# Performance work log

Hardware: AMD Instinct MI355X
Metric: run time of the kernel (lower is better)

The kernel has to match this reference:

```python
import jax, jax.numpy as jnp
import numpy as np

N = 4096  # matrix dimension; M=N, useFrame=False => nCols=N, nThetas=N*(N-1)/2


def _schedule(n):
    """Round-robin tournament schedule: n-1 rounds of n/2 disjoint (i,j) pairs
    covering all i<j exactly once, plus the canonical row-major theta index
    t(i,j) = i*n - i*(i+1)/2 + (j-i-1)."""
    assert n % 2 == 0
    ks = np.arange(1, n // 2)
    i_rounds, j_rounds, t_rounds = [], [], []
    for r in range(n - 1):
        a = np.concatenate(([n - 1], (r + ks) % (n - 1)))
        b = np.concatenate(([r % (n - 1)], (r - ks) % (n - 1)))
        i = np.minimum(a, b)
        j = np.maximum(a, b)
        t = i * n - (i * (i + 1)) // 2 + (j - i - 1)
        i_rounds.append(i)
        j_rounds.append(j)
        t_rounds.append(t)
    return (np.stack(i_rounds).astype(np.int32),
            np.stack(j_rounds).astype(np.int32),
            np.stack(t_rounds).astype(np.int32))


def setup_inputs() -> dict:
    key = jax.random.key(0)
    n_thetas = N * (N - 1) // 2
    # torch.nn.init.uniform_(thetas, 0, 2*pi)
    thetas = jax.random.uniform(key, (n_thetas,), jnp.float32, 0.0, 2.0 * float(np.pi))
    ri, rj, rt = _schedule(N)
    return {
        "thetas": thetas,
        "round_i": jnp.asarray(ri),      # [N-1, N/2]
        "round_j": jnp.asarray(rj),      # [N-1, N/2]
        "round_theta": jnp.asarray(rt),  # [N-1, N/2]
    }


def reference(thetas, round_i, round_j, round_theta):
    # Compose all N(N-1)/2 Givens rotations into U (left-multiplying identity).
    # Within each tournament round the N/2 pairs are disjoint, so rotations
    # commute and can be applied as one vectorized 2-row update.
    n = round_i.shape[0] + 1
    th = thetas[round_theta]            # [R, n/2]
    cs = jnp.cos(th)
    sn = jnp.sin(th)
    U0 = jnp.eye(n, dtype=thetas.dtype)

    def step(U, xs):
        i, j, c, s = xs                 # each [n/2] (c,s) or [n/2] int (i,j)
        Ui = U[i]                       # [n/2, n]
        Uj = U[j]                       # [n/2, n]
        U = U.at[i].set(c[:, None] * Ui - s[:, None] * Uj)
        U = U.at[j].set(s[:, None] * Ui + c[:, None] * Uj)
        return U, None

    U, _ = jax.lax.scan(step, U0, (round_i, round_j, cs, sn))
    return U  # nCols = N (useFrame=False) -> full matrix
```

## Files before the change

### kernel.cpp

```cpp
#include <hip/hip_runtime.h>
#include <math.h>

#define NDIM 4096
#define NR   4095
#define NPAIRS 2048
#define CB   8
#define NTHREADS 256
#define NWAVES (NTHREADS / 64)
#define TPT  8

__global__ void cs_precompute(const float* __restrict__ thetas,
                              const int* __restrict__ round_theta,
                              float2* __restrict__ cs, int total) {
    int idx = blockIdx.x * blockDim.x + threadIdx.x;
    if (idx >= total) return;
    int r = idx / NPAIRS;
    int k = idx - r * NPAIRS;
    float th = thetas[round_theta[idx]];
    float s, c;
    sincosf(th, &s, &c);
    if (k > 0 && k <= r && r < NR - k) s = -s;
    cs[idx] = make_float2(c, s);
}

#define XBAR()                                                          \
  { asm volatile("s_waitcnt lgkmcnt(0)" ::: "memory");                  \
    __builtin_amdgcn_s_barrier(); }

#define PIN8(A, U)                                                      \
    asm volatile("" :: "v"(A[U][0]), "v"(A[U][1]), "v"(A[U][2]),        \
                       "v"(A[U][3]), "v"(A[U][4]), "v"(A[U][5]),        \
                       "v"(A[U][6]), "v"(A[U][7]))

#define PINALL()                                                        \
  { PIN8(T, 0); PIN8(T, 1); PIN8(T, 2); PIN8(T, 3);                     \
    PIN8(T, 4); PIN8(T, 5); PIN8(T, 6); PIN8(T, 7);                     \
    PIN8(B, 0); PIN8(B, 1); PIN8(B, 2); PIN8(B, 3);                     \
    PIN8(B, 4); PIN8(B, 5); PIN8(B, 6); PIN8(B, 7); }

#define UPD(U, P, CC, SS)                                                     \
  { const float c_ = (CC), s_ = (SS);                                         \
    _Pragma("unroll") for (int c = 0; c < CB; ++c) {                          \
      float a = T[((U) + (P)) & 7][c], b = B[((U) - (P) + 8) & 7][c];         \
      T[((U) + (P)) & 7][c] = fmaf(c_, a, -(s_ * b));                         \
      B[((U) - (P) + 8) & 7][c] = fmaf(s_, a, c_ * b); } }

#define PHASE(P, RND, BUF, DO_PF)                                             \
  {                                                                           \
    PINALL();                                                                 \
    float na0[CB], nb0[CB], nbL[CB];                                          \
    {             \
      const float c_ = BUF[0].x, s_ = BUF[0].y;                               \
      _Pragma("unroll") for (int c = 0; c < CB; ++c) {                        \
        float a = T[(P) & 7][c], b = B[(0 - (P) + 8) & 7][c];                 \
        na0[c] = fmaf(c_, a, -(s_ * b));                                      \
        nb0[c] = fmaf(s_, a, c_ * b); } }                                     \
    float t7[CB];                                                             \
    _Pragma("unroll") for (int c = 0; c < CB; ++c)                            \
      t7[c] = __shfl_down(na0[c], 1);       \
    UPD(1, P, BUF[0].z, BUF[0].w)                                             \
    UPD(2, P, BUF[1].x, BUF[1].y)                                             \
    UPD(3, P, BUF[1].z, BUF[1].w)                                             \
    UPD(4, P, BUF[2].x, BUF[2].y)                                             \
    UPD(5, P, BUF[2].z, BUF[2].w)                                             \
    UPD(6, P, BUF[3].x, BUF[3].y)                                             \
    {                                \
      const float c_ = BUF[3].z, s_ = BUF[3].w;                               \
      _Pragma("unroll") for (int c = 0; c < CB; ++c) {                        \
        float a = T[(7 + (P)) & 7][c], b = B[(7 - (P) + 8) & 7][c];           \
        T[(7 + (P)) & 7][c] = fmaf(c_, a, -(s_ * b));                         \
        nbL[c] = fmaf(s_, a, c_ * b); } }                                     \
    if (DO_PF) {     \
      const float4* pf_ = csp + (size_t)((RND) + 2) * (NPAIRS / 2);           \
      BUF[0] = pf_[0]; BUF[1] = pf_[1]; BUF[2] = pf_[2]; BUF[3] = pf_[3];     \
    }                                                                         \
    float bi[CB];                                                             \
    _Pragma("unroll") for (int c = 0; c < CB; ++c)                            \
      bi[c] = __shfl_up(nbL[c], 1);                                           \
    if (lane == 0) { _Pragma("unroll") for (int c = 0; c < CB; ++c)           \
        naBuf[(P) & 1][wave][c] = na0[c]; }                                   \
    if (lane == 63) { _Pragma("unroll") for (int c = 0; c < CB; ++c)          \
        nbBuf[(P) & 1][wave][c] = nbL[c]; }                                   \
    XBAR();                                                                   \
    if (lane == 63) {                                                         \
      if (wave < NWAVES - 1) { _Pragma("unroll")                              \
        for (int c = 0; c < CB; ++c) t7[c] = naBuf[(P) & 1][wave + 1][c]; }   \
      else { _Pragma("unroll")                                                \
        for (int c = 0; c < CB; ++c) t7[c] = nbL[c]; } }                      \
    if (lane == 0 && wave > 0) { _Pragma("unroll")                            \
      for (int c = 0; c < CB; ++c) bi[c] = nbBuf[(P) & 1][wave - 1][c]; }     \
    _Pragma("unroll") for (int c = 0; c < CB; ++c) {                          \
      T[(P) & 7][c] = t7[c];                             \
      B[(0 - (P) + 8) & 7][c] = (tid == 0) ? na0[c] : nb0[c];                 \
      B[(7 - (P) + 8) & 7][c] = (tid == 0) ? nb0[c] : bi[c];                  \
    }                                                                         \
  }

__global__ __launch_bounds__(NTHREADS, 2)
void rotmat_systolic(const float2* __restrict__ cs,
                     float* __restrict__ out) {
    __shared__ float naBuf[2][NWAVES][CB];
    __shared__ float nbBuf[2][NWAVES][CB];

    const int tid  = threadIdx.x;
    const int lane = tid & 63;
    const int wave = tid >> 6;
    const int col0 = blockIdx.x * CB;

    float T[TPT][CB], B[TPT][CB];
#pragma unroll
    for (int u = 0; u < TPT; ++u) {
        int g = tid * TPT + u;
        int rowB = NR - g;
#pragma unroll
        for (int c = 0; c < CB; ++c) {
            T[u][c] = (g == col0 + c) ? 1.f : 0.f;
            B[u][c] = (rowB == col0 + c) ? 1.f : 0.f;
        }
    }

    const float4* csp = (const float4*)cs + (size_t)tid * (TPT / 2);
    float4 csbE[4], csbO[4];
    { const float4* p = csp;
      csbE[0] = p[0]; csbE[1] = p[1]; csbE[2] = p[2]; csbE[3] = p[3]; }
    { const float4* p = csp + (size_t)1 * (NPAIRS / 2);
      csbO[0] = p[0]; csbO[1] = p[1]; csbO[2] = p[2]; csbO[3] = p[3]; }

    int r = 0;
    for (int it = 0; it < 511; ++it, r += 8) {
        PHASE(0, r,     csbE, 1)
        PHASE(1, r + 1, csbO, 1)
        PHASE(2, r + 2, csbE, 1)
        PHASE(3, r + 3, csbO, 1)
        PHASE(4, r + 4, csbE, 1)
        PHASE(5, r + 5, csbO, 1)
        PHASE(6, r + 6, csbE, 1)
        PHASE(7, r + 7, csbO, 1)
    }
    PHASE(0, r,     csbE, 1)
    PHASE(1, r + 1, csbO, 1)
    PHASE(2, r + 2, csbE, 1)
    PHASE(3, r + 3, csbO, 1)
    PHASE(4, r + 4, csbE, 1)
    PHASE(5, r + 5, csbO, 0)
    PHASE(6, r + 6, csbE, 0)

#pragma unroll
    for (int u = 0; u < TPT; ++u) {
        int g = tid * TPT + u;
        int rowB = NR - g;
        float* Tp = T[(u + 7) & 7];
        float* Bp = B[(u + 1) & 7];
        float4* oT = (float4*)&out[(size_t)g * NDIM + col0];
        oT[0] = make_float4(Tp[0], Tp[1], Tp[2], Tp[3]);
        oT[1] = make_float4(Tp[4], Tp[5], Tp[6], Tp[7]);
        float4* oB = (float4*)&out[(size_t)rowB * NDIM + col0];
        oB[0] = make_float4(Bp[0], Bp[1], Bp[2], Bp[3]);
        oB[1] = make_float4(Bp[4], Bp[5], Bp[6], Bp[7]);
    }
}

extern "C" void kernel_launch(void* const* d_in, const int* in_sizes, int n_in,
                              void* d_out, int out_size, void* d_ws, size_t ws_size,
                              hipStream_t stream) {
    const float* thetas      = (const float*)d_in[0];
    const int*   round_theta = (const int*)d_in[3];
    float*       out         = (float*)d_out;

    const int total = NR * NPAIRS;
    float2* cs = (float2*)d_ws;

    cs_precompute<<<(total + 255) / 256, 256, 0, stream>>>(
        thetas, round_theta, cs, total);
    rotmat_systolic<<<NDIM / CB, NTHREADS, 0, stream>>>(cs, out);
}
```

Before: 4.104 ms.

## Overlap cross-wave halo exchange with compute by recomputing boundary rotations locally

Boundary lanes now read the neighbouring wave's values from shared memory at the start of each phase, before the barrier-dependent work. They then recompute the halo rotation locally using a prefetched cos/sin pair and the saved previous value. The barrier moves to the end of the phase, after the next round's boundary values are written, so the LDS round trip is no longer on the critical path between the edge rotations and the shuffle fixup. This costs extra registers (prevX, hst, hcs), a per-phase scalar cos/sin load for the edge lanes, and more complex boundary logic that could be wrong.

New measurement: 15.47 ms. 277% more time.

```diff
diff --git a/kernel.cpp b/kernel.cpp
--- a/kernel.cpp
+++ b/kernel.cpp
@@ -45,9 +45,16 @@
       T[((U) + (P)) & 7][c] = fmaf(c_, a, -(s_ * b));                         \
       B[((U) - (P) + 8) & 7][c] = fmaf(s_, a, c_ * b); } }
 
-#define PHASE(P, RND, BUF, DO_PF)                                             \
+#define PHASE(P, RND, BUF, DO_PF, DO_PH)                                      \
   {                                                                           \
     PINALL();                                                                 \
+    float hst[CB];      \
+    if (lane == 63 && wave < NWAVES - 1) {                                    \
+      _Pragma("unroll") for (int c = 0; c < CB; ++c)                          \
+        hst[c] = naS[(RND) & 1][wave + 1][c]; }                               \
+    if (lane == 0 && wave > 0) {                                              \
+      _Pragma("unroll") for (int c = 0; c < CB; ++c)                          \
+        hst[c] = nbS[(RND) & 1][wave - 1][c]; }                               \
     float na0[CB], nb0[CB], nbL[CB];                                          \
     {             \
       const float c_ = BUF[0].x, s_ = BUF[0].y;                               \
@@ -55,52 +62,58 @@
         float a = T[(P) & 7][c], b = B[(0 - (P) + 8) & 7][c];                 \
         na0[c] = fmaf(c_, a, -(s_ * b));                                      \
         nb0[c] = fmaf(s_, a, c_ * b); } }                                     \
-    float t7[CB];                                                             \
-    _Pragma("unroll") for (int c = 0; c < CB; ++c)                            \
-      t7[c] = __shfl_down(na0[c], 1);       \
+    {                          \
+      const float c_ = BUF[3].z, s_ = BUF[3].w;                               \
+      _Pragma("unroll") for (int c = 0; c < CB; ++c) {                        \
+        float a = T[(7 + (P)) & 7][c], b = B[(7 - (P) + 8) & 7][c];           \
+        T[(7 + (P)) & 7][c] = fmaf(c_, a, -(s_ * b));                         \
+        nbL[c] = fmaf(s_, a, c_ * b); } }                                     \
+    float t7[CB], bi[CB];                                                     \
+    _Pragma("unroll") for (int c = 0; c < CB; ++c) {                          \
+      t7[c] = __shfl_down(na0[c], 1);                                         \
+      bi[c] = __shfl_up(nbL[c], 1); }                                         \
+    if (lane == 63) {                       \
+      _Pragma("unroll") for (int c = 0; c < CB; ++c)                          \
+        t7[c] = (wave == NWAVES - 1) ? nbL[c]                                 \
+                : fmaf(hcs.x, hst[c], -(hcs.y * prevX[c])); }                 \
+    if (lane == 0 && wave > 0) {            \
+      _Pragma("unroll") for (int c = 0; c < CB; ++c)                          \
+        bi[c] = fmaf(hcs.y, prevX[c], hcs.x * hst[c]); }                      \
     UPD(1, P, BUF[0].z, BUF[0].w)                                             \
     UPD(2, P, BUF[1].x, BUF[1].y)                                             \
     UPD(3, P, BUF[1].z, BUF[1].w)                                             \
     UPD(4, P, BUF[2].x, BUF[2].y)                                             \
     UPD(5, P, BUF[2].z, BUF[2].w)                                             \
     UPD(6, P, BUF[3].x, BUF[3].y)                                             \
-    {                                \
-      const float c_ = BUF[3].z, s_ = BUF[3].w;                               \
-      _Pragma("unroll") for (int c = 0; c < CB; ++c) {                        \
-        float a = T[(7 + (P)) & 7][c], b = B[(7 - (P) + 8) & 7][c];           \
-        T[(7 + (P)) & 7][c] = fmaf(c_, a, -(s_ * b));                         \
-        nbL[c] = fmaf(s_, a, c_ * b); } }                                     \
-    if (DO_PF) {     \
+    if (DO_PF) {                \
       const float4* pf_ = csp + (size_t)((RND) + 2) * (NPAIRS / 2);           \
       BUF[0] = pf_[0]; BUF[1] = pf_[1]; BUF[2] = pf_[2]; BUF[3] = pf_[3];     \
     }                                                                         \
-    float bi[CB];                                                             \
+    float2 hn;                                                                \
+    if (DO_PH) { if (lane == 0 || lane == 63)                                 \
+        hn = cs2[(size_t)((RND) + 1) * NPAIRS + hidx]; }                      \
     _Pragma("unroll") for (int c = 0; c < CB; ++c)                            \
-      bi[c] = __shfl_up(nbL[c], 1);                                           \
-    if (lane == 0) { _Pragma("unroll") for (int c = 0; c < CB; ++c)           \
-        naBuf[(P) & 1][wave][c] = na0[c]; }                                   \
-    if (lane == 63) { _Pragma("unroll") for (int c = 0; c < CB; ++c)          \
-        nbBuf[(P) & 1][wave][c] = nbL[c]; }                                   \
-    XBAR();                                                                   \
-    if (lane == 63) {                                                         \
-      if (wave < NWAVES - 1) { _Pragma("unroll")                              \
-        for (int c = 0; c < CB; ++c) t7[c] = naBuf[(P) & 1][wave + 1][c]; }   \
-      else { _Pragma("unroll")                                                \
-        for (int c = 0; c < CB; ++c) t7[c] = nbL[c]; } }                      \
-    if (lane == 0 && wave > 0) { _Pragma("unroll")                            \
-      for (int c = 0; c < CB; ++c) bi[c] = nbBuf[(P) & 1][wave - 1][c]; }     \
+      prevX[c] = (lane == 0) ? na0[c] : nbL[c];                               \
     _Pragma("unroll") for (int c = 0; c < CB; ++c) {                          \
       T[(P) & 7][c] = t7[c];                             \
       B[(0 - (P) + 8) & 7][c] = (tid == 0) ? na0[c] : nb0[c];                 \
       B[(7 - (P) + 8) & 7][c] = (tid == 0) ? nb0[c] : bi[c];                  \
     }                                                                         \
+    if (lane == 0) {                \
+      _Pragma("unroll") for (int c = 0; c < CB; ++c)                          \
+        naS[((RND) + 1) & 1][wave][c] = T[(1 + (P)) & 7][c]; }                \
+    if (lane == 63) {               \
+      _Pragma("unroll") for (int c = 0; c < CB; ++c)                          \
+        nbS[((RND) + 1) & 1][wave][c] = B[(6 - (P) + 8) & 7][c]; }            \
+    if (DO_PH) hcs = hn;                                                      \
+    XBAR();                                                                   \
   }
 
 __global__ __launch_bounds__(NTHREADS, 2)
 void rotmat_systolic(const float2* __restrict__ cs,
                      float* __restrict__ out) {
-    __shared__ float naBuf[2][NWAVES][CB];
-    __shared__ float nbBuf[2][NWAVES][CB];
+    __shared__ float naS[2][NWAVES][CB];
+    __shared__ float nbS[2][NWAVES][CB];
 
     const int tid  = threadIdx.x;
     const int lane = tid & 63;
@@ -120,30 +133,54 @@
     }
 
     const float4* csp = (const float4*)cs + (size_t)tid * (TPT / 2);
+    const float2* cs2 = cs;
     float4 csbE[4], csbO[4];
     { const float4* p = csp;
       csbE[0] = p[0]; csbE[1] = p[1]; csbE[2] = p[2]; csbE[3] = p[3]; }
     { const float4* p = csp + (size_t)1 * (NPAIRS / 2);
       csbO[0] = p[0]; csbO[1] = p[1]; csbO[2] = p[2]; csbO[3] = p[3]; }
 
+    const int hidx = (lane == 63)
+        ? ((tid + 1) * TPT < NPAIRS ? (tid + 1) * TPT : NPAIRS - 1)
+        : (tid * TPT - 1 > 0 ? tid * TPT - 1 : 0);
+    float2 hcs;
+    if (lane == 0 || lane == 63) hcs = cs2[hidx];
+
+    float prevX[CB];
+    {
+        int rowPrev = (lane == 63) ? (NR - (tid + 1) * TPT) : (tid * TPT - 1);
+#pragma unroll
+        for (int c = 0; c < CB; ++c)
+            prevX[c] = (rowPrev == col0 + c) ? 1.f : 0.f;
+    }
+    if (lane == 0) {
+#pragma unroll
+        for (int c = 0; c < CB; ++c) naS[0][wave][c] = T[0][c];
+    }
+    if (lane == 63) {
+#pragma unroll
+        for (int c = 0; c < CB; ++c) nbS[0][wave][c] = B[7][c];
+    }
+    __syncthreads();
+
     int r = 0;
     for (int it = 0; it < 511; ++it, r += 8) {
-        PHASE(0, r,     csbE, 1)
-        PHASE(1, r + 1, csbO, 1)
-        PHASE(2, r + 2, csbE, 1)
-        PHASE(3, r + 3, csbO, 1)
-        PHASE(4, r + 4, csbE, 1)
-        PHASE(5, r + 5, csbO, 1)
-        PHASE(6, r + 6, csbE, 1)
-        PHASE(7, r + 7, csbO, 1)
-    }
-    PHASE(0, r,     csbE, 1)
-    PHASE(1, r + 1, csbO, 1)
-    PHASE(2, r + 2, csbE, 1)
-    PHASE(3, r + 3, csbO, 1)
-    PHASE(4, r + 4, csbE, 1)
-    PHASE(5, r + 5, csbO, 0)
-    PHASE(6, r + 6, csbE, 0)
+        PHASE(0, r,     csbE, 1, 1)
+        PHASE(1, r + 1, csbO, 1, 1)
+        PHASE(2, r + 2, csbE, 1, 1)
+        PHASE(3, r + 3, csbO, 1, 1)
+        PHASE(4, r + 4, csbE, 1, 1)
+        PHASE(5, r + 5, csbO, 1, 1)
+        PHASE(6, r + 6, csbE, 1, 1)
+        PHASE(7, r + 7, csbO, 1, 1)
+    }
+    PHASE(0, r,     csbE, 1, 1)
+    PHASE(1, r + 1, csbO, 1, 1)
+    PHASE(2, r + 2, csbE, 1, 1)
+    PHASE(3, r + 3, csbO, 1, 1)
+    PHASE(4, r + 4, csbE, 1, 1)
+    PHASE(5, r + 5, csbO, 0, 1)
+    PHASE(6, r + 6, csbE, 0, 0)
 
 #pragma unroll
     for (int u = 0; u < TPT; ++u) {
```
